# Optimization experiments

Measured on AMD Instinct MI355X. Metric: run time of the kernel, lower is better.

The kernel has to match this reference:

```python
import jax, jax.numpy as jnp
import numpy as np

B, N, D, H = 2, 2048, 1024, 16
HD = D // H  # head_dim = 64


def l2norm(x, eps=1e-12):
    n = jnp.sqrt(jnp.sum(x * x, axis=-1, keepdims=True))
    return x / jnp.maximum(n, eps)


def setup_inputs() -> dict:
    key = jax.random.key(0)
    ks = jax.random.split(key, 10)
    s = 0.02
    return {
        "x": jax.random.normal(ks[0], (B, N, D), jnp.float32),
        "Wq": jax.random.normal(ks[1], (D, D), jnp.float32) * s,
        "Wk": jax.random.normal(ks[2], (D, D), jnp.float32) * s,
        "Wv": jax.random.normal(ks[3], (D, D), jnp.float32) * s,
        "Wgamma": jax.random.normal(ks[4], (D, H), jnp.float32) * s,
        "Wf": jax.random.normal(ks[5], (D, H), jnp.float32) * s,
        "Wg1": jax.random.normal(ks[6], (D, HD), jnp.float32) * s,
        "Wg2": jax.random.normal(ks[7], (HD, D), jnp.float32) * s,
        "Wo": jax.random.normal(ks[8], (D, D), jnp.float32) * s,
        "norm_w": jnp.ones((D,), jnp.float32),
    }


def dplr_delta_rule(q, k, v, a, gk):
    # q,k,v,a,gk: (B,N,H,HD). State S: (B,H,Dk,Dv). b-vector == k here.
    # S' = S * exp(gk_t); S_t = S' + k_t (x) (a_t @ S' + v_t); o_t = q_t @ S_t
    qm, km, vm, am, gm = (jnp.moveaxis(t, 1, 0) for t in (q, k, v, a, gk))

    def step(S, inp):
        qt, kt, vt, at, gkt = inp  # (B,H,HD)
        Sp = S * jnp.exp(gkt)[..., None]
        u = jnp.einsum('bhk,bhkv->bhv', at, Sp) + vt
        S = Sp + jnp.einsum('bhk,bhv->bhkv', kt, u)
        o = jnp.einsum('bhk,bhkv->bhv', qt, S)
        return S, o

    S0 = jnp.zeros((q.shape[0], q.shape[2], q.shape[3], v.shape[3]), q.dtype)
    _, o = jax.lax.scan(step, S0, (qm, km, vm, am, gm))
    return jnp.moveaxis(o, 0, 1)  # (B,N,H,HD)


def _forward(x, Wq, Wk, Wv, Wgamma, Wf, Wg1, Wg2, Wo, norm_w):
    b, n, d = x.shape
    silu = jax.nn.silu
    q = silu(x @ Wq)
    k = silu(x @ Wk)
    v = silu(x @ Wv)
    log_f = jax.nn.log_sigmoid(x @ Wf)          # (b,n,H) scalar decay per head
    gamma = -jax.nn.sigmoid(x @ Wgamma)         # (b,n,H), 'pos' activation
    q = q.reshape(b, n, H, HD)
    k = l2norm(k.reshape(b, n, H, HD))
    v = v.reshape(b, n, H, HD)
    gk = jnp.broadcast_to(log_f[..., None], (b, n, H, HD))  # repeat over head_dim
    a = k * gamma[..., None] * jnp.exp(gk)
    out = dplr_delta_rule(q, k, v, a, gk)       # scale=1
    out = out.reshape(b, n, d)
    gate = jax.nn.sigmoid((x @ Wg1) @ Wg2)
    out = out * gate
    # LayerNorm (weight only, no bias)
    mu = jnp.mean(out, axis=-1, keepdims=True)
    var = jnp.mean(jnp.square(out - mu), axis=-1, keepdims=True)
    out = (out - mu) * jax.lax.rsqrt(var + 1e-5) * norm_w
    return out @ Wo


def reference(x, Wq, Wk, Wv, Wgamma, Wf, Wg1, Wg2, Wo, norm_w):
    return _forward(x, Wq, Wk, Wv, Wgamma, Wf, Wg1, Wg2, Wo, norm_w)
```

## Files before the change

### kernel.cpp

```cpp
#include <hip/hip_runtime.h>

#define BB 2
#define NN 2048
#define DD 1024
#define HH 16
#define HD 64
#define RR (BB * NN)
#define CT 32
#define NC (NN / CT)

typedef __bf16 bf16x8 __attribute__((ext_vector_type(8)));
typedef __bf16 bf16x4 __attribute__((ext_vector_type(4)));
typedef float f32x4 __attribute__((ext_vector_type(4)));
typedef float f32x2 __attribute__((ext_vector_type(2)));

__device__ __forceinline__ float sigmoidf_(float x) { return 1.f / (1.f + __expf(-x)); }

#define MFMA16(a, b, c) __builtin_amdgcn_mfma_f32_16x16x32_bf16((a), (b), (c), 0, 0, 0)

__device__ __forceinline__ void gl2lds16(const void* g, void* l) {
    __builtin_amdgcn_global_load_lds((const __attribute__((address_space(1))) void*)g,
                                     (__attribute__((address_space(3))) void*)l, 16, 0, 0);
}

__global__ __launch_bounds__(256) void xcvt(const float* __restrict__ x,
                                            __bf16* __restrict__ xb) {
    const size_t i = ((size_t)blockIdx.x * 256 + threadIdx.x) * 8;
    float4 a = *(const float4*)(x + i);
    float4 b = *(const float4*)(x + i + 4);
    bf16x8 o;
    o[0] = (__bf16)a.x; o[1] = (__bf16)a.y; o[2] = (__bf16)a.z; o[3] = (__bf16)a.w;
    o[4] = (__bf16)b.x; o[5] = (__bf16)b.y; o[6] = (__bf16)b.z; o[7] = (__bf16)b.w;
    *(bf16x8*)(xb + i) = o;
}

__global__ __launch_bounds__(256) void wtrans(const float* S0, const float* S1,
                                              const float* S2, const float* S3,
                                              __bf16* D0, __bf16* D1,
                                              __bf16* D2, __bf16* D3,
                                              int K, int N) {
    __shared__ float t[64][65];
    const int z = blockIdx.z;
    const float* S = (z == 0) ? S0 : ((z == 1) ? S1 : ((z == 2) ? S2 : S3));
    __bf16* D = (z == 0) ? D0 : ((z == 1) ? D1 : ((z == 2) ? D2 : D3));
    const int tid = threadIdx.x;
    const int ti = blockIdx.y * 64;
    const int tj = blockIdx.x * 64;
    const int r = tid >> 2, c0 = (tid & 3) * 16;
    const float* sp = S + (size_t)(ti + r) * N + tj + c0;
#pragma unroll
    for (int p = 0; p < 4; p++) {
        float4 v = *(const float4*)(sp + 4 * p);
        t[r][c0 + 4 * p + 0] = v.x; t[r][c0 + 4 * p + 1] = v.y;
        t[r][c0 + 4 * p + 2] = v.z; t[r][c0 + 4 * p + 3] = v.w;
    }
    __syncthreads();
    bf16x8 o0, o1;
#pragma unroll
    for (int j = 0; j < 8; j++) o0[j] = (__bf16)t[c0 + j][r];
#pragma unroll
    for (int j = 0; j < 8; j++) o1[j] = (__bf16)t[c0 + 8 + j][r];
    __bf16* dp = D + (size_t)(tj + r) * K + ti + c0;
    *(bf16x8*)dp = o0;
    *(bf16x8*)(dp + 8) = o1;
}

__global__ __launch_bounds__(256) void wtrans96(const float* __restrict__ Wgm,
                                                const float* __restrict__ Wf,
                                                const float* __restrict__ Wg1,
                                                __bf16* __restrict__ W96T) {
    const int c = blockIdx.x;
    const int k0 = threadIdx.x * 4;
    bf16x4 o;
    if (c < 96) {
        const float* src;
        int stride;
        if (c < 16)      { src = Wgm + c;        stride = 16; }
        else if (c < 32) { src = Wf + (c - 16);  stride = 16; }
        else             { src = Wg1 + (c - 32); stride = 64; }
#pragma unroll
        for (int j = 0; j < 4; j++) o[j] = (__bf16)src[(size_t)(k0 + j) * stride];
    } else {
        o[0] = o[1] = o[2] = o[3] = (__bf16)0.f;
    }
    *(bf16x4*)(W96T + (size_t)c * 1024 + k0) = o;
}

__global__ __launch_bounds__(256) void gemm_bt(const __bf16* __restrict__ A,
                                               const __bf16* B0, const __bf16* B1,
                                               const __bf16* B2, const __bf16* B3,
                                               float* C0, float* C1, float* C2, float* C3,
                                               int M, int N, int K) {
    constexpr int BK = 32;
    __shared__ __align__(16) __bf16 As[128 * BK];
    __shared__ __align__(16) __bf16 Bs[128 * BK];
    const int mat = blockIdx.x >> 3;
    const __bf16* B = (mat == 0) ? B0 : ((mat == 1) ? B1 : ((mat == 2) ? B2 : B3));
    float* C = (mat == 0) ? C0 : ((mat == 1) ? C1 : ((mat == 2) ? C2 : C3));
    const int Nn = (mat == 3) ? 128 : N;
    const int tid = threadIdx.x;
    const int lane = tid & 63;
    const int wave = tid >> 6;
    const int wm = (wave >> 1) * 64, wn = (wave & 1) * 64;
    const int bm = blockIdx.y * 128, bn = (blockIdx.x & 7) * 128;
    const int l15 = lane & 15, quad = lane >> 4;

    const int srow = lane >> 2, scol = (lane & 3) * 8;
    const __bf16* gA = A + (size_t)(bm + wave * 16 + srow) * K + scol;
    const __bf16* gB = B + (size_t)(bn + wave * 16 + srow) * K + scol;
    const size_t rstep = (size_t)64 * K;
    __bf16* lA0 = &As[(wave * 16) * BK];
    __bf16* lA1 = &As[(wave * 16 + 64) * BK];
    __bf16* lB0 = &Bs[(wave * 16) * BK];
    __bf16* lB1 = &Bs[(wave * 16 + 64) * BK];

    f32x4 acc[4][4];
#pragma unroll
    for (int i = 0; i < 4; i++)
#pragma unroll
        for (int j = 0; j < 4; j++) acc[i][j] = (f32x4){0.f, 0.f, 0.f, 0.f};

    gl2lds16(gA, lA0);
    gl2lds16(gA + rstep, lA1);
    gl2lds16(gB, lB0);
    gl2lds16(gB + rstep, lB1);

    for (int kb = 0; kb < K; kb += BK) {
        asm volatile("s_waitcnt vmcnt(0)" ::: "memory");
        __syncthreads();

        bf16x8 af[4], bfr[4];
#pragma unroll
        for (int i = 0; i < 4; i++)
            af[i] = *(const bf16x8*)&As[(wm + i * 16 + l15) * BK + quad * 8];
#pragma unroll
        for (int j = 0; j < 4; j++)
            bfr[j] = *(const bf16x8*)&Bs[(wn + j * 16 + l15) * BK + quad * 8];
        __syncthreads();

        if (kb + BK < K) {
            gl2lds16(gA + kb + BK, lA0);
            gl2lds16(gA + kb + BK + rstep, lA1);
            gl2lds16(gB + kb + BK, lB0);
            gl2lds16(gB + kb + BK + rstep, lB1);
        }
        __builtin_amdgcn_sched_barrier(0);

#pragma unroll
        for (int i = 0; i < 4; i++)
#pragma unroll
            for (int j = 0; j < 4; j++)
                acc[i][j] = MFMA16(af[i], bfr[j], acc[i][j]);
    }

#pragma unroll
    for (int i = 0; i < 4; i++) {
#pragma unroll
        for (int r = 0; r < 4; r++) {
            const int row = bm + wm + i * 16 + quad * 4 + r;
            float* cp = C + (size_t)row * Nn + bn + wn + l15;
#pragma unroll
            for (int j = 0; j < 4; j++) cp[j * 16] = acc[i][j][r];
        }
    }
}

__global__ __launch_bounds__(256) void scal_prep(const float* __restrict__ c96,
                                                 float* __restrict__ lfb,
                                                 float* __restrict__ csb,
                                                 __bf16* __restrict__ g1b) {
    const int tid = threadIdx.x;
    const int row = blockIdx.x * 16 + (tid >> 4);
    const int h = tid & 15;
    const float* cr = c96 + (size_t)row * 128;
    const float sig = sigmoidf_(cr[16 + h]);
    const float gm = -sigmoidf_(cr[h]);
    lfb[(size_t)row * HH + h] = sig;
    csb[(size_t)row * HH + h] = gm * sig * sig;
    const int c4 = h * 4;
    bf16x4 o;
    o[0] = (__bf16)cr[32 + c4 + 0]; o[1] = (__bf16)cr[32 + c4 + 1];
    o[2] = (__bf16)cr[32 + c4 + 2]; o[3] = (__bf16)cr[32 + c4 + 3];
    *(bf16x4*)(g1b + (size_t)row * 64 + c4) = o;
}

__global__ __launch_bounds__(64) void chunk_prep(const float* __restrict__ qb,
                                                 const float* __restrict__ kb,
                                                 const float* __restrict__ lfb,
                                                 const float* __restrict__ csb,
                                                 __bf16* __restrict__ ck_hat,
                                                 __bf16* __restrict__ ck_q,
                                                 __bf16* __restrict__ ck_kbT,
                                                 __bf16* __restrict__ ck_M,
                                                 __bf16* __restrict__ ck_G,
                                                 float* __restrict__ ck_lam) {
    __shared__ __align__(16) __bf16 khL[32][72];
    __shared__ __align__(16) __bf16 kbL[32][72];
    __shared__ __align__(16) __bf16 qtL[32][72];
    __shared__ float Afp[32][33];
    __shared__ float scl[3][32];
    const int bx = blockIdx.x;
    const int bh = bx >> 6, ci = bx & 63;
    const int b = bh >> 4, h = bh & 15;
    const int l = threadIdx.x;
    const int l15 = l & 15, quad = l >> 4, t32 = l & 31;
    const size_t cid = (size_t)bh * NC + ci;

    const size_t mb = ((size_t)(b * NN + ci * CT) + t32) * HH + h;
    float c_t = csb[mb];
    float p = lfb[mb];
#pragma unroll
    for (int d = 1; d <= 16; d <<= 1) {
        float o = __shfl_up(p, d);
        p *= (t32 >= d) ? o : 1.f;
    }
    float pm1 = __shfl_up(p, 1);
    if (t32 == 0) pm1 = 1.f;
    const float lamT = __shfl(p, 31);
    if (l < 32) {
        scl[0][t32] = c_t * pm1;
        scl[1][t32] = 1.f / p;
        scl[2][t32] = p;
    }
    if (l == 0) ck_lam[cid] = lamT;
    __syncthreads();

    const size_t rb0 = ((size_t)(b * NN + ci * CT)) * DD + h * HD;
    __bf16* khG = ck_hat + cid * 2048;
    __bf16* qtG = ck_q + cid * 2048;
    __bf16* kTG = ck_kbT + cid * 2048;
#pragma unroll
    for (int rep = 0; rep < 8; rep++) {
        const int row = rep * 4 + quad;
        const int c4 = l15 * 4;
        float4 kv = *(const float4*)(kb + rb0 + (size_t)row * DD + c4);
        float4 qv = *(const float4*)(qb + rb0 + (size_t)row * DD + c4);
        kv.x *= sigmoidf_(kv.x); kv.y *= sigmoidf_(kv.y);
        kv.z *= sigmoidf_(kv.z); kv.w *= sigmoidf_(kv.w);
        qv.x *= sigmoidf_(qv.x); qv.y *= sigmoidf_(qv.y);
        qv.z *= sigmoidf_(qv.z); qv.w *= sigmoidf_(qv.w);
        float ss = kv.x * kv.x + kv.y * kv.y + kv.z * kv.z + kv.w * kv.w;
        ss += __shfl_xor(ss, 1); ss += __shfl_xor(ss, 2);
        ss += __shfl_xor(ss, 4); ss += __shfl_xor(ss, 8);
        const float inv = 1.f / fmaxf(sqrtf(ss), 1e-12f);
        const float sh = scl[0][row] * inv, sbr = scl[1][row] * inv, sq = scl[2][row];
        bf16x4 khv, kbv, qtv;
        khv[0] = (__bf16)(kv.x * sh); khv[1] = (__bf16)(kv.y * sh);
        khv[2] = (__bf16)(kv.z * sh); khv[3] = (__bf16)(kv.w * sh);
        kbv[0] = (__bf16)(kv.x * sbr); kbv[1] = (__bf16)(kv.y * sbr);
        kbv[2] = (__bf16)(kv.z * sbr); kbv[3] = (__bf16)(kv.w * sbr);
        qtv[0] = (__bf16)(qv.x * sq); qtv[1] = (__bf16)(qv.y * sq);
        qtv[2] = (__bf16)(qv.z * sq); qtv[3] = (__bf16)(qv.w * sq);
        *(bf16x4*)&khL[row][c4] = khv;
        *(bf16x4*)&kbL[row][c4] = kbv;
        *(bf16x4*)&qtL[row][c4] = qtv;
        *(bf16x4*)(khG + row * 64 + c4) = khv;
        *(bf16x4*)(qtG + row * 64 + c4) = qtv;
#pragma unroll
        for (int j = 0; j < 4; j++) kTG[(c4 + j) * 32 + row] = kbv[j];
    }
    __syncthreads();

    __bf16* GG = ck_G + cid * 1024;
#pragma unroll
    for (int mi = 0; mi < 2; mi++)
#pragma unroll
        for (int ni = 0; ni < 2; ni++) {
            f32x4 aA = (f32x4){0.f, 0.f, 0.f, 0.f};
            f32x4 aG = (f32x4){0.f, 0.f, 0.f, 0.f};
#pragma unroll
            for (int k2 = 0; k2 < 2; k2++) {
                bf16x8 bfr = *(const bf16x8*)&kbL[ni * 16 + l15][k2 * 32 + quad * 8];
                bf16x8 afr = *(const bf16x8*)&khL[mi * 16 + l15][k2 * 32 + quad * 8];
                bf16x8 qfr = *(const bf16x8*)&qtL[mi * 16 + l15][k2 * 32 + quad * 8];
                aA = MFMA16(afr, bfr, aA);
                aG = MFMA16(qfr, bfr, aG);
            }
#pragma unroll
            for (int r = 0; r < 4; r++) {
                const int row = mi * 16 + quad * 4 + r, col = ni * 16 + l15;
                Afp[row][col] = (col < row) ? aA[r] : 0.f;
                GG[row * 32 + col] = (__bf16)((col <= row) ? aG[r] : 0.f);
            }
        }
    __syncthreads();

    __bf16* MG = ck_M + cid * 1024;
    if (l < 32) {
        float m[32];
#pragma unroll
        for (int t = 0; t < 32; t++) {
            float r = (l == t) ? 1.f : 0.f;
#pragma unroll
            for (int s = 0; s < t; s++) r += Afp[t][s] * m[s];
            m[t] = r;
            MG[t * 32 + l] = (__bf16)r;
        }
    }
}

struct FragSet {
    bf16x8 ka[2][2], qa[2][2], ma[2], ga[2], kba[4];
    f32x4 vv[2];
    float lam;
};

__global__ __launch_bounds__(64) void chunk_scan(const __bf16* __restrict__ ck_hat,
                                                 const __bf16* __restrict__ ck_q,
                                                 const __bf16* __restrict__ ck_kbT,
                                                 const __bf16* __restrict__ ck_M,
                                                 const __bf16* __restrict__ ck_G,
                                                 const float* __restrict__ ck_lam,
                                                 const float* __restrict__ vb,
                                                 __bf16* __restrict__ obh) {
    __shared__ __align__(16) __bf16 Sbt[16][72];
    __shared__ __align__(16) __bf16 Vbt[16][40];
    __shared__ __align__(16) __bf16 Ubt[16][40];
    const int bx = blockIdx.x;
    const int bh = bx >> 2, vs = bx & 3;
    const int b = bh >> 4, h = bh & 15;
    const int l = threadIdx.x, l15 = l & 15, quad = l >> 4;
    const size_t cid0 = (size_t)bh * NC;
    const size_t vcol = (size_t)h * HD + vs * 16 + l15;
    const size_t rowb = (size_t)b * NN;

    f32x4 S[4];
#pragma unroll
    for (int dt = 0; dt < 4; dt++) S[dt] = (f32x4){0.f, 0.f, 0.f, 0.f};

    auto load = [&](FragSet& f, int ci) {
        const __bf16* khp = ck_hat + (cid0 + ci) * 2048;
        const __bf16* qp = ck_q + (cid0 + ci) * 2048;
        const __bf16* kTp = ck_kbT + (cid0 + ci) * 2048;
        const __bf16* Mp = ck_M + (cid0 + ci) * 1024;
        const __bf16* Gp = ck_G + (cid0 + ci) * 1024;
#pragma unroll
        for (int mi = 0; mi < 2; mi++) {
#pragma unroll
            for (int k2 = 0; k2 < 2; k2++) {
                f.ka[mi][k2] = *(const bf16x8*)(khp + (mi * 16 + l15) * 64 + k2 * 32 + quad * 8);
                f.qa[mi][k2] = *(const bf16x8*)(qp + (mi * 16 + l15) * 64 + k2 * 32 + quad * 8);
            }
            f.ma[mi] = *(const bf16x8*)(Mp + (mi * 16 + l15) * 32 + quad * 8);
            f.ga[mi] = *(const bf16x8*)(Gp + (mi * 16 + l15) * 32 + quad * 8);
        }
#pragma unroll
        for (int dt = 0; dt < 4; dt++)
            f.kba[dt] = *(const bf16x8*)(kTp + (dt * 16 + l15) * 32 + quad * 8);
#pragma unroll
        for (int mi = 0; mi < 2; mi++)
#pragma unroll
            for (int r = 0; r < 4; r++)
                f.vv[mi][r] = vb[(rowb + ci * CT + mi * 16 + quad * 4 + r) * DD + vcol];
        f.lam = ck_lam[cid0 + ci];
    };

    auto compute = [&](const FragSet& f, int ci) {
        const f32x4 z = (f32x4){0.f, 0.f, 0.f, 0.f};
#pragma unroll
        for (int dt = 0; dt < 4; dt++) {
            bf16x4 t;
#pragma unroll
            for (int r = 0; r < 4; r++) t[r] = (__bf16)S[dt][r];
            *(bf16x4*)&Sbt[l15][dt * 16 + quad * 4] = t;
        }
        bf16x8 sb0 = *(const bf16x8*)&Sbt[l15][quad * 8];
        bf16x8 sb1 = *(const bf16x8*)&Sbt[l15][32 + quad * 8];
        f32x4 p0 = MFMA16(f.ka[0][0], sb0, z); p0 = MFMA16(f.ka[0][1], sb1, p0);
        f32x4 p1 = MFMA16(f.ka[1][0], sb0, z); p1 = MFMA16(f.ka[1][1], sb1, p1);
#pragma unroll
        for (int r = 0; r < 4; r++) {
            const float v0 = f.vv[0][r], v1 = f.vv[1][r];
            p0[r] += v0 * sigmoidf_(v0);
            p1[r] += v1 * sigmoidf_(v1);
        }
        bf16x4 t0, t1;
#pragma unroll
        for (int r = 0; r < 4; r++) { t0[r] = (__bf16)p0[r]; t1[r] = (__bf16)p1[r]; }
        *(bf16x4*)&Vbt[l15][quad * 4] = t0;
        *(bf16x4*)&Vbt[l15][16 + quad * 4] = t1;
        bf16x8 vfr = *(const bf16x8*)&Vbt[l15][quad * 8];
        f32x4 u0 = MFMA16(f.ma[0], vfr, z);
        f32x4 u1 = MFMA16(f.ma[1], vfr, z);
#pragma unroll
        for (int r = 0; r < 4; r++) { t0[r] = (__bf16)u0[r]; t1[r] = (__bf16)u1[r]; }
        *(bf16x4*)&Ubt[l15][quad * 4] = t0;
        *(bf16x4*)&Ubt[l15][16 + quad * 4] = t1;
        bf16x8 ufr = *(const bf16x8*)&Ubt[l15][quad * 8];
        f32x4 o0 = MFMA16(f.qa[0][0], sb0, z); o0 = MFMA16(f.qa[0][1], sb1, o0);
        o0 = MFMA16(f.ga[0], ufr, o0);
        f32x4 o1 = MFMA16(f.qa[1][0], sb0, z); o1 = MFMA16(f.qa[1][1], sb1, o1);
        o1 = MFMA16(f.ga[1], ufr, o1);
#pragma unroll
        for (int r = 0; r < 4; r++) {
            obh[(rowb + ci * CT + quad * 4 + r) * DD + vcol] = (__bf16)o0[r];
            obh[(rowb + ci * CT + 16 + quad * 4 + r) * DD + vcol] = (__bf16)o1[r];
        }
#pragma unroll
        for (int dt = 0; dt < 4; dt++) {
            S[dt] = MFMA16(f.kba[dt], ufr, S[dt]);
#pragma unroll
            for (int r = 0; r < 4; r++) S[dt][r] *= f.lam;
        }
    };

    FragSet fA, fB;
    load(fA, 0);
    for (int ci = 0; ci < NC; ci += 2) {
        load(fB, ci + 1);
        __builtin_amdgcn_sched_barrier(0);
        compute(fA, ci);
        load(fA, (ci + 2 < NC) ? ci + 2 : NC - 1);
        __builtin_amdgcn_sched_barrier(0);
        compute(fB, ci + 1);
    }
}

__global__ __launch_bounds__(256) void gate_ln_kernel(const __bf16* __restrict__ obh,
                                                      const float* __restrict__ gatep,
                                                      const float* __restrict__ nw,
                                                      __bf16* __restrict__ lnob) {
    const int r = blockIdx.x, tid = threadIdx.x;
    const int wav = tid >> 6, lane = tid & 63;
    __shared__ float red[8];
    const size_t rb = (size_t)r * DD;

    float vals[4];
    float s = 0.f;
#pragma unroll
    for (int p = 0; p < 4; p++) {
        const int j = tid + 256 * p;
        float xg = (float)obh[rb + j] * sigmoidf_(gatep[rb + j]);
        vals[p] = xg;
        s += xg;
    }
#pragma unroll
    for (int m = 1; m <= 32; m <<= 1) s += __shfl_xor(s, m);
    if (lane == 0) red[wav] = s;
    __syncthreads();
    const float mu = (red[0] + red[1] + red[2] + red[3]) * (1.f / 1024.f);

    float s2 = 0.f;
#pragma unroll
    for (int p = 0; p < 4; p++) { float d = vals[p] - mu; s2 += d * d; }
#pragma unroll
    for (int m = 1; m <= 32; m <<= 1) s2 += __shfl_xor(s2, m);
    if (lane == 0) red[4 + wav] = s2;
    __syncthreads();
    const float var = (red[4] + red[5] + red[6] + red[7]) * (1.f / 1024.f);
    const float rs = rsqrtf(var + 1e-5f);

#pragma unroll
    for (int p = 0; p < 4; p++) {
        const int j = tid + 256 * p;
        lnob[rb + j] = (__bf16)((vals[p] - mu) * rs * nw[j]);
    }
}

extern "C" void kernel_launch(void* const* d_in, const int* in_sizes, int n_in,
                              void* d_out, int out_size, void* d_ws, size_t ws_size,
                              hipStream_t stream) {
    const float* x   = (const float*)d_in[0];
    const float* Wq  = (const float*)d_in[1];
    const float* Wk  = (const float*)d_in[2];
    const float* Wv  = (const float*)d_in[3];
    const float* Wgm = (const float*)d_in[4];
    const float* Wf  = (const float*)d_in[5];
    const float* Wg1 = (const float*)d_in[6];
    const float* Wg2 = (const float*)d_in[7];
    const float* Wo  = (const float*)d_in[8];
    const float* nw  = (const float*)d_in[9];
    float* out = (float*)d_out;

    float* w = (float*)d_ws;
    float* qb    = w;
    float* kb    = qb + 4194304;
    float* vb    = kb + 4194304;
    float* gatep = vb + 4194304;
    __bf16* g1b  = (__bf16*)(gatep + 4194304);
    float* lfb   = gatep + 4194304 + 131072;
    float* csb   = lfb + 65536;
    __bf16* obh  = (__bf16*)(csb + 65536);
    float* cw    = csb + 65536 + 2097152;
    __bf16* ck_hat = (__bf16*)cw;
    __bf16* ck_q   = (__bf16*)(cw + 2097152);
    __bf16* ck_kbT = (__bf16*)(cw + 4194304);
    __bf16* ck_M   = (__bf16*)(cw + 6291456);
    __bf16* ck_G   = (__bf16*)(cw + 7340032);
    float*  ck_lam = cw + 8388608;
    float* nw2   = cw + 8390656;
    __bf16* xb   = (__bf16*)nw2;
    __bf16* WqT  = (__bf16*)(nw2 + 2097152);
    __bf16* WkT  = (__bf16*)(nw2 + 2621440);
    __bf16* WvT  = (__bf16*)(nw2 + 3145728);
    __bf16* WoT  = (__bf16*)(nw2 + 3670016);
    __bf16* Wg2T = (__bf16*)(nw2 + 4194304);
    __bf16* W96T = (__bf16*)(nw2 + 4227072);
    float* c96   = nw2 + 4292608;
    __bf16* lnob = (__bf16*)qb;

    dim3 blk(256);
    xcvt<<<2048, blk, 0, stream>>>(x, xb);
    wtrans<<<dim3(16, 16, 4), blk, 0, stream>>>(Wq, Wk, Wv, Wo, WqT, WkT, WvT, WoT,
                                                DD, DD);
    wtrans<<<dim3(16, 1, 1), blk, 0, stream>>>(Wg2, Wg2, Wg2, Wg2, Wg2T, Wg2T, Wg2T,
                                               Wg2T, HD, DD);
    wtrans96<<<128, blk, 0, stream>>>(Wgm, Wf, Wg1, W96T);
    gemm_bt<<<dim3(25, 32), blk, 0, stream>>>(xb, WqT, WkT, WvT, W96T,
                                              qb, kb, vb, c96, RR, DD, DD);
    scal_prep<<<RR / 16, blk, 0, stream>>>(c96, lfb, csb, g1b);
    gemm_bt<<<dim3(8, 32), blk, 0, stream>>>(g1b, Wg2T, Wg2T, Wg2T, Wg2T,
                                             gatep, gatep, gatep, gatep, RR, DD, HD);
    chunk_prep<<<32 * NC, 64, 0, stream>>>(qb, kb, lfb, csb,
                                           ck_hat, ck_q, ck_kbT, ck_M, ck_G, ck_lam);
    chunk_scan<<<128, 64, 0, stream>>>(ck_hat, ck_q, ck_kbT, ck_M, ck_G, ck_lam, vb, obh);
    gate_ln_kernel<<<RR, blk, 0, stream>>>(obh, gatep, nw, lnob);
    gemm_bt<<<dim3(8, 32), blk, 0, stream>>>(lnob, WoT, WoT, WoT, WoT,
                                             out, out, out, out, RR, DD, DD);
}
```

Baseline: 258.5 us.

## Swizzle GEMM block order and process two value slices per scan wave

The GEMM kernel remaps its flat block index with a stride-8 swizzle, likely to spread neighbouring workgroups across XCDs and improve L2 locality. The chunk scan kernel now has each 64-thread block handle two 16-column value slices instead of one. The per-chunk key/query/M/G fragments are loaded once and shared by both slices, and independent MFMA chains are interleaved to hide latency. This halves the scan grid to 64 blocks and raises register use per wave, which cuts parallelism on a latency-bound serial kernel.

```diff
diff --git a/kernel.cpp b/kernel.cpp
--- a/kernel.cpp
+++ b/kernel.cpp
@@ -94,7 +94,11 @@
     constexpr int BK = 32;
     __shared__ __align__(16) __bf16 As[128 * BK];
     __shared__ __align__(16) __bf16 Bs[128 * BK];
-    const int mat = blockIdx.x >> 3;
+    const int nwg = (int)(gridDim.x * gridDim.y);
+    const int flat = (int)(blockIdx.y * gridDim.x + blockIdx.x);
+    const int swz = (flat & 7) * (nwg >> 3) + (flat >> 3);
+    const int bxs = swz % (int)gridDim.x, bys = swz / (int)gridDim.x;
+    const int mat = bxs >> 3;
     const __bf16* B = (mat == 0) ? B0 : ((mat == 1) ? B1 : ((mat == 2) ? B2 : B3));
     float* C = (mat == 0) ? C0 : ((mat == 1) ? C1 : ((mat == 2) ? C2 : C3));
     const int Nn = (mat == 3) ? 128 : N;
@@ -102,7 +106,7 @@
     const int lane = tid & 63;
     const int wave = tid >> 6;
     const int wm = (wave >> 1) * 64, wn = (wave & 1) * 64;
-    const int bm = blockIdx.y * 128, bn = (blockIdx.x & 7) * 128;
+    const int bm = bys * 128, bn = (bxs & 7) * 128;
     const int l15 = lane & 15, quad = lane >> 4;
 
     const int srow = lane >> 2, scol = (lane & 3) * 8;
@@ -301,7 +305,7 @@
 
 struct FragSet {
     bf16x8 ka[2][2], qa[2][2], ma[2], ga[2], kba[4];
-    f32x4 vv[2];
+    f32x4 vv[2][2];
     float lam;
 };
 
@@ -313,20 +317,23 @@
                                                  const float* __restrict__ ck_lam,
                                                  const float* __restrict__ vb,
                                                  __bf16* __restrict__ obh) {
-    __shared__ __align__(16) __bf16 Sbt[16][72];
-    __shared__ __align__(16) __bf16 Vbt[16][40];
-    __shared__ __align__(16) __bf16 Ubt[16][40];
+    __shared__ __align__(16) __bf16 Sbt[2][16][72];
+    __shared__ __align__(16) __bf16 Vbt[2][16][40];
+    __shared__ __align__(16) __bf16 Ubt[2][16][40];
     const int bx = blockIdx.x;
-    const int bh = bx >> 2, vs = bx & 3;
+    const int bh = bx >> 1, pp = bx & 1;
     const int b = bh >> 4, h = bh & 15;
     const int l = threadIdx.x, l15 = l & 15, quad = l >> 4;
     const size_t cid0 = (size_t)bh * NC;
-    const size_t vcol = (size_t)h * HD + vs * 16 + l15;
+    const size_t vcol[2] = {(size_t)h * HD + (size_t)(pp * 2) * 16 + l15,
+                            (size_t)h * HD + (size_t)(pp * 2 + 1) * 16 + l15};
     const size_t rowb = (size_t)b * NN;
 
-    f32x4 S[4];
-#pragma unroll
-    for (int dt = 0; dt < 4; dt++) S[dt] = (f32x4){0.f, 0.f, 0.f, 0.f};
+    f32x4 S[2][4];
+#pragma unroll
+    for (int s = 0; s < 2; s++)
+#pragma unroll
+        for (int dt = 0; dt < 4; dt++) S[s][dt] = (f32x4){0.f, 0.f, 0.f, 0.f};
 
     auto load = [&](FragSet& f, int ci) {
         const __bf16* khp = ck_hat + (cid0 + ci) * 2048;
@@ -348,60 +355,95 @@
         for (int dt = 0; dt < 4; dt++)
             f.kba[dt] = *(const bf16x8*)(kTp + (dt * 16 + l15) * 32 + quad * 8);
 #pragma unroll
-        for (int mi = 0; mi < 2; mi++)
-#pragma unroll
-            for (int r = 0; r < 4; r++)
-                f.vv[mi][r] = vb[(rowb + ci * CT + mi * 16 + quad * 4 + r) * DD + vcol];
+        for (int s = 0; s < 2; s++)
+#pragma unroll
+            for (int mi = 0; mi < 2; mi++)
+#pragma unroll
+                for (int r = 0; r < 4; r++)
+                    f.vv[s][mi][r] =
+                        vb[(rowb + ci * CT + mi * 16 + quad * 4 + r) * DD + vcol[s]];
         f.lam = ck_lam[cid0 + ci];
     };
 
     auto compute = [&](const FragSet& f, int ci) {
         const f32x4 z = (f32x4){0.f, 0.f, 0.f, 0.f};
 #pragma unroll
-        for (int dt = 0; dt < 4; dt++) {
-            bf16x4 t;
-#pragma unroll
-            for (int r = 0; r < 4; r++) t[r] = (__bf16)S[dt][r];
-            *(bf16x4*)&Sbt[l15][dt * 16 + quad * 4] = t;
-        }
-        bf16x8 sb0 = *(const bf16x8*)&Sbt[l15][quad * 8];
-        bf16x8 sb1 = *(const bf16x8*)&Sbt[l15][32 + quad * 8];
-        f32x4 p0 = MFMA16(f.ka[0][0], sb0, z); p0 = MFMA16(f.ka[0][1], sb1, p0);
-        f32x4 p1 = MFMA16(f.ka[1][0], sb0, z); p1 = MFMA16(f.ka[1][1], sb1, p1);
-#pragma unroll
-        for (int r = 0; r < 4; r++) {
-            const float v0 = f.vv[0][r], v1 = f.vv[1][r];
-            p0[r] += v0 * sigmoidf_(v0);
-            p1[r] += v1 * sigmoidf_(v1);
-        }
-        bf16x4 t0, t1;
-#pragma unroll
-        for (int r = 0; r < 4; r++) { t0[r] = (__bf16)p0[r]; t1[r] = (__bf16)p1[r]; }
-        *(bf16x4*)&Vbt[l15][quad * 4] = t0;
-        *(bf16x4*)&Vbt[l15][16 + quad * 4] = t1;
-        bf16x8 vfr = *(const bf16x8*)&Vbt[l15][quad * 8];
-        f32x4 u0 = MFMA16(f.ma[0], vfr, z);
-        f32x4 u1 = MFMA16(f.ma[1], vfr, z);
-#pragma unroll
-        for (int r = 0; r < 4; r++) { t0[r] = (__bf16)u0[r]; t1[r] = (__bf16)u1[r]; }
-        *(bf16x4*)&Ubt[l15][quad * 4] = t0;
-        *(bf16x4*)&Ubt[l15][16 + quad * 4] = t1;
-        bf16x8 ufr = *(const bf16x8*)&Ubt[l15][quad * 8];
-        f32x4 o0 = MFMA16(f.qa[0][0], sb0, z); o0 = MFMA16(f.qa[0][1], sb1, o0);
-        o0 = MFMA16(f.ga[0], ufr, o0);
-        f32x4 o1 = MFMA16(f.qa[1][0], sb0, z); o1 = MFMA16(f.qa[1][1], sb1, o1);
-        o1 = MFMA16(f.ga[1], ufr, o1);
-#pragma unroll
-        for (int r = 0; r < 4; r++) {
-            obh[(rowb + ci * CT + quad * 4 + r) * DD + vcol] = (__bf16)o0[r];
-            obh[(rowb + ci * CT + 16 + quad * 4 + r) * DD + vcol] = (__bf16)o1[r];
-        }
-#pragma unroll
-        for (int dt = 0; dt < 4; dt++) {
-            S[dt] = MFMA16(f.kba[dt], ufr, S[dt]);
-#pragma unroll
-            for (int r = 0; r < 4; r++) S[dt][r] *= f.lam;
-        }
+        for (int s = 0; s < 2; s++)
+#pragma unroll
+            for (int dt = 0; dt < 4; dt++) {
+                bf16x4 t;
+#pragma unroll
+                for (int r = 0; r < 4; r++) t[r] = (__bf16)S[s][dt][r];
+                *(bf16x4*)&Sbt[s][l15][dt * 16 + quad * 4] = t;
+            }
+        bf16x8 sb0[2], sb1[2];
+#pragma unroll
+        for (int s = 0; s < 2; s++) {
+            sb0[s] = *(const bf16x8*)&Sbt[s][l15][quad * 8];
+            sb1[s] = *(const bf16x8*)&Sbt[s][l15][32 + quad * 8];
+        }
+        f32x4 p0[2], p1[2];
+#pragma unroll
+        for (int s = 0; s < 2; s++) {
+            p0[s] = MFMA16(f.ka[0][0], sb0[s], z); p0[s] = MFMA16(f.ka[0][1], sb1[s], p0[s]);
+            p1[s] = MFMA16(f.ka[1][0], sb0[s], z); p1[s] = MFMA16(f.ka[1][1], sb1[s], p1[s]);
+        }
+#pragma unroll
+        for (int s = 0; s < 2; s++)
+#pragma unroll
+            for (int r = 0; r < 4; r++) {
+                const float v0 = f.vv[s][0][r], v1 = f.vv[s][1][r];
+                p0[s][r] += v0 * sigmoidf_(v0);
+                p1[s][r] += v1 * sigmoidf_(v1);
+            }
+#pragma unroll
+        for (int s = 0; s < 2; s++) {
+            bf16x4 t0, t1;
+#pragma unroll
+            for (int r = 0; r < 4; r++) { t0[r] = (__bf16)p0[s][r]; t1[r] = (__bf16)p1[s][r]; }
+            *(bf16x4*)&Vbt[s][l15][quad * 4] = t0;
+            *(bf16x4*)&Vbt[s][l15][16 + quad * 4] = t1;
+        }
+        bf16x8 vfr[2];
+#pragma unroll
+        for (int s = 0; s < 2; s++) vfr[s] = *(const bf16x8*)&Vbt[s][l15][quad * 8];
+        f32x4 u0[2], u1[2];
+#pragma unroll
+        for (int s = 0; s < 2; s++) {
+            u0[s] = MFMA16(f.ma[0], vfr[s], z);
+            u1[s] = MFMA16(f.ma[1], vfr[s], z);
+        }
+#pragma unroll
+        for (int s = 0; s < 2; s++) {
+            bf16x4 t0, t1;
+#pragma unroll
+            for (int r = 0; r < 4; r++) { t0[r] = (__bf16)u0[s][r]; t1[r] = (__bf16)u1[s][r]; }
+            *(bf16x4*)&Ubt[s][l15][quad * 4] = t0;
+            *(bf16x4*)&Ubt[s][l15][16 + quad * 4] = t1;
+        }
+        bf16x8 ufr[2];
+#pragma unroll
+        for (int s = 0; s < 2; s++) ufr[s] = *(const bf16x8*)&Ubt[s][l15][quad * 8];
+#pragma unroll
+        for (int s = 0; s < 2; s++) {
+            f32x4 o0 = MFMA16(f.qa[0][0], sb0[s], z); o0 = MFMA16(f.qa[0][1], sb1[s], o0);
+            o0 = MFMA16(f.ga[0], ufr[s], o0);
+            f32x4 o1 = MFMA16(f.qa[1][0], sb0[s], z); o1 = MFMA16(f.qa[1][1], sb1[s], o1);
+            o1 = MFMA16(f.ga[1], ufr[s], o1);
+#pragma unroll
+            for (int r = 0; r < 4; r++) {
+                obh[(rowb + ci * CT + quad * 4 + r) * DD + vcol[s]] = (__bf16)o0[r];
+                obh[(rowb + ci * CT + 16 + quad * 4 + r) * DD + vcol[s]] = (__bf16)o1[r];
+            }
+        }
+#pragma unroll
+        for (int s = 0; s < 2; s++)
+#pragma unroll
+            for (int dt = 0; dt < 4; dt++) {
+                S[s][dt] = MFMA16(f.kba[dt], ufr[s], S[s][dt]);
+#pragma unroll
+                for (int r = 0; r < 4; r++) S[s][dt][r] *= f.lam;
+            }
     };
 
     FragSet fA, fB;
@@ -513,7 +555,7 @@
                                              gatep, gatep, gatep, gatep, RR, DD, HD);
     chunk_prep<<<32 * NC, 64, 0, stream>>>(qb, kb, lfb, csb,
                                            ck_hat, ck_q, ck_kbT, ck_M, ck_G, ck_lam);
-    chunk_scan<<<128, 64, 0, stream>>>(ck_hat, ck_q, ck_kbT, ck_M, ck_G, ck_lam, vb, obh);
+    chunk_scan<<<64, 64, 0, stream>>>(ck_hat, ck_q, ck_kbT, ck_M, ck_G, ck_lam, vb, obh);
     gate_ln_kernel<<<RR, blk, 0, stream>>>(obh, gatep, nw, lnob);
     gemm_bt<<<dim3(8, 32), blk, 0, stream>>>(lnob, WoT, WoT, WoT, WoT,
                                              out, out, out, out, RR, DD, DD);
```

After: 294.4 us. +13.9%, slower.
